# Kernel optimization log

Hardware: AMD Instinct MI355X
Metric: run time of the kernel (lower is better)

## Reference

```python
import jax, jax.numpy as jnp
import numpy as np

B, C, H, W = 64, 1, 1024, 1024
NEG_WEIGHT = 0.1  # constant loss contribution where target != 1


def setup_inputs() -> dict:
    key = jax.random.key(0)
    k1, k2 = jax.random.split(key)
    prediction = jax.random.normal(k1, (B, C, H, W), dtype=jnp.float32)
    target = jax.random.randint(k2, (B, C, H, W), 0, 2, dtype=jnp.int32)
    return {"prediction": prediction, "target": target}


def reference(prediction, target):
    # loss_i = 1 - sigmoid(pred_i) if target_i == 1 else 0.1; return mean over all elements
    p = jax.nn.sigmoid(prediction)
    loss = jnp.where(target == 1, 1.0 - p, jnp.float32(NEG_WEIGHT))
    return jnp.mean(loss)
```

## Files before the change

### kernel.cpp

```cpp
#include <hip/hip_runtime.h>


#define BLOCK 256

__device__ __forceinline__ float loss4(float4 p, int4 t) {
    float l0 = (t.x == 1) ? 1.0f / (1.0f + __expf(p.x)) : 0.1f;
    float l1 = (t.y == 1) ? 1.0f / (1.0f + __expf(p.y)) : 0.1f;
    float l2 = (t.z == 1) ? 1.0f / (1.0f + __expf(p.z)) : 0.1f;
    float l3 = (t.w == 1) ? 1.0f / (1.0f + __expf(p.w)) : 0.1f;
    return (l0 + l1) + (l2 + l3);
}

__device__ __forceinline__ void block_reduce_atomic(float acc, float inv_n,
                                                    float* __restrict__ out) {
#pragma unroll
    for (int off = 32; off > 0; off >>= 1)
        acc += __shfl_down(acc, off, 64);
    __shared__ float smem[BLOCK / 64];
    const int lane = threadIdx.x & 63;
    const int wave = threadIdx.x >> 6;
    if (lane == 0) smem[wave] = acc;
    __syncthreads();
    if (threadIdx.x == 0) {
        float bsum = (smem[0] + smem[1]) + (smem[2] + smem[3]);
        atomicAdd(out, bsum * inv_n);
    }
}

__global__ __launch_bounds__(BLOCK)
void wloss_pipe(const float4* __restrict__ p4,
                const int4*   __restrict__ t4,
                float* __restrict__ out,
                int iters, int stride, float inv_n) {
    int i = blockIdx.x * BLOCK + threadIdx.x;

    float4 pA = p4[i];          int4 tA = t4[i];
    float4 pB = p4[i + stride]; int4 tB = t4[i + stride];
    int idx = i + 2 * stride;

    float acc = 0.0f;
    for (int k = 0; k < iters - 2; ++k) {
        float4 pN = p4[idx];
        int4   tN = t4[idx];
        idx += stride;
        acc += loss4(pA, tA);
        pA = pB; tA = tB;
        pB = pN; tB = tN;
    }
    acc += loss4(pA, tA);
    acc += loss4(pB, tB);

    block_reduce_atomic(acc, inv_n, out);
}

__global__ __launch_bounds__(BLOCK)
void wloss_generic(const float* __restrict__ pred,
                   const int*   __restrict__ tgt,
                   float* __restrict__ out,
                   long long n, float inv_n) {
    const long long n4     = n >> 2;
    const long long tid    = (long long)blockIdx.x * blockDim.x + threadIdx.x;
    const long long stride = (long long)gridDim.x * blockDim.x;

    const float4* p4 = (const float4*)pred;
    const int4*   t4 = (const int4*)tgt;

    float acc = 0.0f;
    for (long long i = tid; i < n4; i += stride)
        acc += loss4(p4[i], t4[i]);
    if (blockIdx.x == 0) {
        for (long long i = (n4 << 2) + threadIdx.x; i < n; i += blockDim.x)
            acc += (tgt[i] == 1) ? 1.0f / (1.0f + __expf(pred[i])) : 0.1f;
    }
    block_reduce_atomic(acc, inv_n, out);
}

extern "C" void kernel_launch(void* const* d_in, const int* in_sizes, int n_in,
                              void* d_out, int out_size, void* d_ws, size_t ws_size,
                              hipStream_t stream) {
    const float* pred = (const float*)d_in[0];
    const int*   tgt  = (const int*)d_in[1];
    float*       out  = (float*)d_out;

    const long long n = (long long)in_sizes[0];
    const float inv_n = 1.0f / (float)n;

    hipMemsetAsync(out, 0, sizeof(float), stream);

    const long long n4 = n >> 2;
    const int grid = 2048;
    const long long stride = (long long)grid * BLOCK;

    if ((n & 3) == 0 && n4 % stride == 0 && n4 / stride >= 2) {
        const int iters = (int)(n4 / stride);
        wloss_pipe<<<grid, BLOCK, 0, stream>>>((const float4*)pred,
                                               (const int4*)tgt, out,
                                               iters, (int)stride, inv_n);
    } else {
        long long g = (n4 + BLOCK - 1) / BLOCK;
        if (g > 8192) g = 8192;
        if (g < 1)    g = 1;
        wloss_generic<<<(int)g, BLOCK, 0, stream>>>(pred, tgt, out, n, inv_n);
    }
}
```

Baseline: 506.5 us.

## Deepen load pipeline to four slots with inline-asm global loads and explicit waitcnt

Replaces the compiler-scheduled two-deep register pipeline with a hand-written four-slot software pipeline. It issues global_load_dwordx4 through inline assembly using a scalar base and a 32-bit vector byte offset, and uses explicit s_waitcnt vmcnt so that eight loads stay in flight per thread. The goal is to keep more memory requests outstanding and raise achieved bandwidth on this streaming reduction. The cost is more live vector registers and a narrower fast-path condition: iterations must be a multiple of four, at least eight, and byte offsets must fit in 31 bits.

```diff
diff --git a/kernel.cpp b/kernel.cpp
--- a/kernel.cpp
+++ b/kernel.cpp
@@ -2,8 +2,12 @@
 
 
 #define BLOCK 256
+#define GRID  2048
 
-__device__ __forceinline__ float loss4(float4 p, int4 t) {
+typedef float vf4 __attribute__((ext_vector_type(4)));
+typedef int   vi4 __attribute__((ext_vector_type(4)));
+
+__device__ __forceinline__ float loss4(vf4 p, vi4 t) {
     float l0 = (t.x == 1) ? 1.0f / (1.0f + __expf(p.x)) : 0.1f;
     float l1 = (t.y == 1) ? 1.0f / (1.0f + __expf(p.y)) : 0.1f;
     float l2 = (t.z == 1) ? 1.0f / (1.0f + __expf(p.z)) : 0.1f;
@@ -27,28 +31,53 @@
     }
 }
 
+#define LOAD_SLOT(P, T)                                                  \
+    asm volatile("global_load_dwordx4 %0, %2, %3\n\t"                    \
+                 "global_load_dwordx4 %1, %2, %4"                        \
+                 : "=&v"(P), "=&v"(T)                                    \
+                 : "v"(off), "s"(pred), "s"(tgt));
+
+#define WAIT_SLOT(N, P, T)                                               \
+    asm volatile("s_waitcnt vmcnt(" #N ")" : "+v"(P), "+v"(T));
+
 __global__ __launch_bounds__(BLOCK)
-void wloss_pipe(const float4* __restrict__ p4,
-                const int4*   __restrict__ t4,
-                float* __restrict__ out,
-                int iters, int stride, float inv_n) {
-    int i = blockIdx.x * BLOCK + threadIdx.x;
+void wloss_asm(const float* __restrict__ pred,
+               const int*   __restrict__ tgt,
+               float* __restrict__ out,
+               int steady, unsigned stride_b, float inv_n) {
+    unsigned off = (blockIdx.x * BLOCK + threadIdx.x) * 16u;
 
-    float4 pA = p4[i];          int4 tA = t4[i];
-    float4 pB = p4[i + stride]; int4 tB = t4[i + stride];
-    int idx = i + 2 * stride;
+    vf4 p0, p1, p2, p3;
+    vi4 t0, t1, t2, t3;
+
+    LOAD_SLOT(p0, t0) off += stride_b;
+    LOAD_SLOT(p1, t1) off += stride_b;
+    LOAD_SLOT(p2, t2) off += stride_b;
+    LOAD_SLOT(p3, t3) off += stride_b;
 
     float acc = 0.0f;
-    for (int k = 0; k < iters - 2; ++k) {
-        float4 pN = p4[idx];
-        int4   tN = t4[idx];
-        idx += stride;
-        acc += loss4(pA, tA);
-        pA = pB; tA = tB;
-        pB = pN; tB = tN;
+    for (int k = 0; k < steady; ++k) {
+        WAIT_SLOT(6, p0, t0)
+        acc += loss4(p0, t0);
+        LOAD_SLOT(p0, t0) off += stride_b;
+
+        WAIT_SLOT(6, p1, t1)
+        acc += loss4(p1, t1);
+        LOAD_SLOT(p1, t1) off += stride_b;
+
+        WAIT_SLOT(6, p2, t2)
+        acc += loss4(p2, t2);
+        LOAD_SLOT(p2, t2) off += stride_b;
+
+        WAIT_SLOT(6, p3, t3)
+        acc += loss4(p3, t3);
+        LOAD_SLOT(p3, t3) off += stride_b;
     }
-    acc += loss4(pA, tA);
-    acc += loss4(pB, tB);
+
+    WAIT_SLOT(6, p0, t0) acc += loss4(p0, t0);
+    WAIT_SLOT(4, p1, t1) acc += loss4(p1, t1);
+    WAIT_SLOT(2, p2, t2) acc += loss4(p2, t2);
+    WAIT_SLOT(0, p3, t3) acc += loss4(p3, t3);
 
     block_reduce_atomic(acc, inv_n, out);
 }
@@ -62,8 +91,8 @@
     const long long tid    = (long long)blockIdx.x * blockDim.x + threadIdx.x;
     const long long stride = (long long)gridDim.x * blockDim.x;
 
-    const float4* p4 = (const float4*)pred;
-    const int4*   t4 = (const int4*)tgt;
+    const vf4* p4 = (const vf4*)pred;
+    const vi4* t4 = (const vi4*)tgt;
 
     float acc = 0.0f;
     for (long long i = tid; i < n4; i += stride)
@@ -88,14 +117,14 @@
     hipMemsetAsync(out, 0, sizeof(float), stream);
 
     const long long n4 = n >> 2;
-    const int grid = 2048;
-    const long long stride = (long long)grid * BLOCK;
+    const long long stride_f4 = (long long)GRID * BLOCK;
+    const long long iters = (n4 > 0 && n4 % stride_f4 == 0) ? n4 / stride_f4 : 0;
 
-    if ((n & 3) == 0 && n4 % stride == 0 && n4 / stride >= 2) {
-        const int iters = (int)(n4 / stride);
-        wloss_pipe<<<grid, BLOCK, 0, stream>>>((const float4*)pred,
-                                               (const int4*)tgt, out,
-                                               iters, (int)stride, inv_n);
+    if ((n & 3) == 0 && iters >= 8 && (iters & 3) == 0 &&
+        (long long)iters * stride_f4 * 16 <= 0x7fffffffLL) {
+        const int steady = (int)(iters / 4 - 1);
+        wloss_asm<<<GRID, BLOCK, 0, stream>>>(pred, tgt, out, steady,
+                                              (unsigned)(stride_f4 * 16), inv_n);
     } else {
         long long g = (n4 + BLOCK - 1) / BLOCK;
         if (g > 8192) g = 8192;
```

Result: slower. 530.8 us (+4.8%).
